# Optimization experiments

Measured on AMD Instinct MI355X. Metric: run time of the kernel, lower is better.

Reference implementation:

```python
import jax, jax.numpy as jnp
import numpy as np

LN_EPS = 1e-5


def setup_inputs() -> dict:
    key = jax.random.key(0)
    ks = jax.random.split(key, 4)
    B, S, D, V, M = 32, 512, 1024, 32000, 77
    X = jax.random.normal(ks[0], (B, S, D), dtype=jnp.float32)
    masked_positions = jax.random.randint(ks[1], (B, M), 0, S, dtype=jnp.int64 if jax.config.jax_enable_x64 else jnp.int32)
    W1 = jax.random.normal(ks[2], (D, D), dtype=jnp.float32) * (1.0 / np.sqrt(D))
    b1 = jnp.zeros((D,), jnp.float32)
    gamma = jnp.ones((D,), jnp.float32)
    beta = jnp.zeros((D,), jnp.float32)
    W2 = jax.random.normal(ks[3], (D, V), dtype=jnp.float32) * (1.0 / np.sqrt(D))
    b2 = jnp.zeros((V,), jnp.float32)
    return {"X": X, "masked_positions": masked_positions, "W1": W1, "b1": b1,
            "gamma": gamma, "beta": beta, "W2": W2, "b2": b2}


def reference(X, masked_positions, W1, b1, gamma, beta, W2, b2):
    # Gather masked token embeddings: X[b, masked_positions[b, m]] -> [B, M, D]
    masked_X = jnp.take_along_axis(X, masked_positions[:, :, None], axis=1)
    # Linear -> ReLU
    h = jax.nn.relu(jnp.einsum('bmd,dh->bmh', masked_X, W1) + b1)
    # LayerNorm over last dim
    mu = jnp.mean(h, axis=-1, keepdims=True)
    var = jnp.mean(jnp.square(h - mu), axis=-1, keepdims=True)
    h = (h - mu) * jax.lax.rsqrt(var + LN_EPS) * gamma + beta
    # Vocab projection
    return jnp.einsum('bmh,hv->bmv', h, W2) + b2
```

## Files before the change

kernel.cpp:

```cpp
#include <hip/hip_runtime.h>
#include <cstdint>

#define D_DIM 1024
#define V_DIM 32000
#define S_DIM 512
#define M_TOK 77
#define ROWS 2464
#define ROWS_PAD 2560

typedef __attribute__((ext_vector_type(8))) short bf16x8;
typedef __attribute__((ext_vector_type(4))) float f32x4;
typedef __attribute__((ext_vector_type(4))) uint16_t u16x4;

__device__ __forceinline__ uint16_t f2bf(float f) {
    union { float f; uint32_t u; } w; w.f = f;
    uint32_t r = (w.u + 0x7FFFu + ((w.u >> 16) & 1u)) >> 16;
    return (uint16_t)r;
}

__device__ __forceinline__ void async_copy16(const uint16_t* g, uint16_t* l) {
    __builtin_amdgcn_global_load_lds((const __attribute__((address_space(1))) void*)g,
                                     (__attribute__((address_space(3))) void*)l,
                                     16, 0, 0);
}

__global__ __launch_bounds__(256) void transpose_f32_bf16(const float* __restrict__ in,
                                                          uint16_t* __restrict__ out,
                                                          int R, int C) {
    __shared__ uint16_t tile[64][65];
    const int c0 = blockIdx.x * 64, r0 = blockIdx.y * 64;
    const int t  = threadIdx.x;
    const int lr = t >> 4;
    const int lc = (t & 15) * 4;
#pragma unroll
    for (int p = 0; p < 4; ++p) {
        const float* src = in + (size_t)(r0 + p * 16 + lr) * C + c0 + lc;
        f32x4 v = *(const f32x4*)src;
        tile[p * 16 + lr][lc + 0] = f2bf(v.x);
        tile[p * 16 + lr][lc + 1] = f2bf(v.y);
        tile[p * 16 + lr][lc + 2] = f2bf(v.z);
        tile[p * 16 + lr][lc + 3] = f2bf(v.w);
    }
    __syncthreads();
#pragma unroll
    for (int p = 0; p < 4; ++p) {
        const int oc = p * 16 + lr;
        u16x4 v;
        v.x = tile[lc + 0][oc];
        v.y = tile[lc + 1][oc];
        v.z = tile[lc + 2][oc];
        v.w = tile[lc + 3][oc];
        *(u16x4*)(out + (size_t)(c0 + oc) * R + r0 + lc) = v;
    }
}

__global__ __launch_bounds__(256) void gather_rows(const float* __restrict__ X,
                                                   const int* __restrict__ pos,
                                                   uint16_t* __restrict__ Ag) {
    const int r = blockIdx.x;
    const int t = threadIdx.x;
    size_t src = 0;
    if (r < ROWS) {
        const int b = r / M_TOK;
        const int p = pos[r];
        src = ((size_t)b * S_DIM + p) * D_DIM;
    }
    f32x4 v = *(const f32x4*)(X + src + t * 4);
    u16x4 o;
    o.x = f2bf(v.x); o.y = f2bf(v.y); o.z = f2bf(v.z); o.w = f2bf(v.w);
    *(u16x4*)(Ag + (size_t)r * D_DIM + t * 4) = o;
}

template <int EPI>
__global__ __launch_bounds__(256, 2) void gemm_bt(const uint16_t* __restrict__ A,
                                                  const uint16_t* __restrict__ B,
                                                  const float* __restrict__ bias,
                                                  float* __restrict__ C,
                                                  int K, int N, int MValid) {
    __shared__ uint16_t As[128 * 64];
    __shared__ uint16_t Bs[128 * 64];
    const int tid  = threadIdx.x;
    const int lane = tid & 63;
    const int wave = tid >> 6;
    const int wr   = (wave >> 1) * 64;
    const int wc   = (wave & 1) * 64;
    const int tM   = blockIdx.y * 128;
    const int tN   = blockIdx.x * 128;
    const int l15  = lane & 15;
    const int l4   = lane >> 4;

    const f32x4 zero = {0.f, 0.f, 0.f, 0.f};
    f32x4 acc[4][4];
#pragma unroll
    for (int i = 0; i < 4; ++i)
#pragma unroll
        for (int j = 0; j < 4; ++j) acc[i][j] = zero;

    const uint16_t* Agp = A + (size_t)(tM + (tid >> 3)) * K + (tid & 7) * 8;
    const uint16_t* Bgp = B + (size_t)(tN + (tid >> 3)) * K + (tid & 7) * 8;
    uint16_t* Asl = &As[tid * 8];
    uint16_t* Bsl = &Bs[tid * 8];
    const size_t rstep = (size_t)32 * K;

    for (int k0 = 0; k0 < K; k0 += 64) {
#pragma unroll
        for (int i = 0; i < 4; ++i)
            async_copy16(Agp + i * rstep + k0, Asl + i * 2048);
#pragma unroll
        for (int i = 0; i < 4; ++i)
            async_copy16(Bgp + i * rstep + k0, Bsl + i * 2048);
        __syncthreads();
#pragma unroll
        for (int kk = 0; kk < 2; ++kk) {
            bf16x8 af[4], bfr[4];
#pragma unroll
            for (int i = 0; i < 4; ++i)
                af[i] = *(const bf16x8*)&As[(wr + i * 16 + l15) * 64 + kk * 32 + l4 * 8];
#pragma unroll
            for (int j = 0; j < 4; ++j)
                bfr[j] = *(const bf16x8*)&Bs[(wc + j * 16 + l15) * 64 + kk * 32 + l4 * 8];
#pragma unroll
            for (int i = 0; i < 4; ++i)
#pragma unroll
                for (int j = 0; j < 4; ++j)
                    acc[i][j] = __builtin_amdgcn_mfma_f32_16x16x32_bf16(af[i], bfr[j],
                                                                        acc[i][j], 0, 0, 0);
        }
        __syncthreads();
    }

#pragma unroll
    for (int j = 0; j < 4; ++j) {
        const int col = tN + wc + j * 16 + l15;
        const float bv = bias[col];
#pragma unroll
        for (int i = 0; i < 4; ++i) {
            const int row0 = tM + wr + i * 16 + l4 * 4;
#pragma unroll
            for (int r = 0; r < 4; ++r) {
                const int row = row0 + r;
                float v = acc[i][j][r] + bv;
                if (EPI == 0) {
                    v = v > 0.f ? v : 0.f;
                    C[(size_t)row * N + col] = v;
                } else {
                    if (row < MValid)
                        C[(size_t)row * N + col] = v;
                }
            }
        }
    }
}

__global__ __launch_bounds__(256) void layernorm_rows(const float* __restrict__ H,
                                                      const float* __restrict__ gamma,
                                                      const float* __restrict__ beta,
                                                      uint16_t* __restrict__ Hn) {
    const int row = blockIdx.x;
    const int t   = threadIdx.x;
    const float* h = H + (size_t)row * D_DIM;
    f32x4 v = *(const f32x4*)(h + t * 4);
    float s  = v.x + v.y + v.z + v.w;
    float sq = v.x * v.x + v.y * v.y + v.z * v.z + v.w * v.w;
#pragma unroll
    for (int o = 32; o > 0; o >>= 1) {
        s  += __shfl_down(s, o, 64);
        sq += __shfl_down(sq, o, 64);
    }
    __shared__ float ss[4], sqs[4];
    if ((t & 63) == 0) { ss[t >> 6] = s; sqs[t >> 6] = sq; }
    __syncthreads();
    const float S    = ss[0] + ss[1] + ss[2] + ss[3];
    const float SQ   = sqs[0] + sqs[1] + sqs[2] + sqs[3];
    const float mean = S * (1.f / D_DIM);
    const float var  = SQ * (1.f / D_DIM) - mean * mean;
    const float rstd = rsqrtf(var + 1e-5f);
    const int c = t * 4;
    f32x4 g = *(const f32x4*)(gamma + c);
    f32x4 bt = *(const f32x4*)(beta + c);
    u16x4 o;
    o.x = f2bf((v.x - mean) * rstd * g.x + bt.x);
    o.y = f2bf((v.y - mean) * rstd * g.y + bt.y);
    o.z = f2bf((v.z - mean) * rstd * g.z + bt.z);
    o.w = f2bf((v.w - mean) * rstd * g.w + bt.w);
    *(u16x4*)(Hn + (size_t)row * D_DIM + c) = o;
}

extern "C" void kernel_launch(void* const* d_in, const int* in_sizes, int n_in,
                              void* d_out, int out_size, void* d_ws, size_t ws_size,
                              hipStream_t stream) {
    const float* X     = (const float*)d_in[0];
    const int*   mp    = (const int*)d_in[1];
    const float* W1    = (const float*)d_in[2];
    const float* b1    = (const float*)d_in[3];
    const float* gamma = (const float*)d_in[4];
    const float* beta  = (const float*)d_in[5];
    const float* W2    = (const float*)d_in[6];
    const float* b2    = (const float*)d_in[7];

    char* ws = (char*)d_ws;
    uint16_t* W2T = (uint16_t*)(ws);
    uint16_t* W1T = (uint16_t*)(ws + 65536000);
    uint16_t* Ag  = (uint16_t*)(ws + 65536000 + 2097152);
    uint16_t* Hn  = (uint16_t*)(ws + 65536000 + 2097152 + 5242880);
    float*    H   = (float*)   (ws + 65536000 + 2097152 + 5242880 + 5242880);

    transpose_f32_bf16<<<dim3(V_DIM / 64, D_DIM / 64), 256, 0, stream>>>(W2, W2T, D_DIM, V_DIM);
    transpose_f32_bf16<<<dim3(D_DIM / 64, D_DIM / 64), 256, 0, stream>>>(W1, W1T, D_DIM, D_DIM);
    gather_rows<<<ROWS_PAD, 256, 0, stream>>>(X, mp, Ag);
    gemm_bt<0><<<dim3(D_DIM / 128, ROWS_PAD / 128), 256, 0, stream>>>(Ag, W1T, b1, H,
                                                                      D_DIM, D_DIM, ROWS_PAD);
    layernorm_rows<<<ROWS_PAD, 256, 0, stream>>>(H, gamma, beta, Hn);
    gemm_bt<1><<<dim3(V_DIM / 128, ROWS_PAD / 128), 256, 0, stream>>>(Hn, W2T, b2, (float*)d_out,
                                                                      D_DIM, V_DIM, ROWS);
}
```

Baseline: 712.9 us.

## Replace vocab GEMM with 256x256 double-buffered, swizzled, XCD-remapped MFMA kernel

Adds a dedicated kernel for the large vocab projection. It uses 256x256 tiles with 8 waves and double-buffered LDS, so global-to-LDS loads of the next K step overlap the current MFMAs. It also adds an XOR swizzle to avoid LDS bank conflicts, remaps workgroups across XCDs for cache locality, and uses setprio around the MFMA bursts. The trade-offs are heavy register pressure (128 accumulator floats per lane) and 128KB of LDS per block, which limits occupancy. The larger tiles also waste more work on padded rows and leave fewer workgroups overall (1250).

Result: faster. 690.6 us (-3.1%).

```diff
diff --git a/kernel.cpp b/kernel.cpp
--- a/kernel.cpp
+++ b/kernel.cpp
@@ -7,6 +7,14 @@
 #define M_TOK 77
 #define ROWS 2464
 #define ROWS_PAD 2560
+
+#define G2_BM 256
+#define G2_BN 256
+#define G2_BK 64
+#define G2_MT (ROWS_PAD / G2_BM)
+#define G2_NT (V_DIM / G2_BN)
+#define G2_NWG (G2_MT * G2_NT)
+#define G2_KT (D_DIM / G2_BK)
 
 typedef __attribute__((ext_vector_type(8))) short bf16x8;
 typedef __attribute__((ext_vector_type(4))) float f32x4;
@@ -152,6 +160,154 @@
     }
 }
 
+__global__ __launch_bounds__(512, 2) void gemm2_256(const uint16_t* __restrict__ A,
+                                                    const uint16_t* __restrict__ B,
+                                                    const float* __restrict__ bias,
+                                                    float* __restrict__ C,
+                                                    int MValid) {
+    __shared__ uint16_t lds[65536];
+    const int tid  = threadIdx.x;
+    const int lane = tid & 63;
+    const int wave = tid >> 6;
+    const int l15  = lane & 15;
+    const int l4   = lane >> 4;
+    const int R0   = (wave >> 2) * 128;
+    const int C0   = (wave & 3) * 64;
+
+    const int bid = blockIdx.x;
+    const int q = G2_NWG >> 3, r = G2_NWG & 7;
+    const int xcd = bid & 7, lin = bid >> 3;
+    const int wg = (xcd < r ? xcd * (q + 1) : r * (q + 1) + (xcd - r) * q) + lin;
+    const int tM = (wg % G2_MT) * G2_BM;
+    const int tN = (wg / G2_MT) * G2_BN;
+
+    const int srow = tid >> 3;
+    const int scel = ((((tid & 7) << 4) ^ ((srow & 7) << 4)) >> 1);
+    const uint16_t* Ags = A + (size_t)(tM + srow) * D_DIM + scel;
+    const uint16_t* Bgs = B + (size_t)(tN + srow) * D_DIM + scel;
+    uint16_t* AsD = &lds[tid * 8];
+    uint16_t* BsD = &lds[16384 + tid * 8];
+
+    const f32x4 zero = {0.f, 0.f, 0.f, 0.f};
+    f32x4 acc[8][4];
+#pragma unroll
+    for (int i = 0; i < 8; ++i)
+#pragma unroll
+        for (int j = 0; j < 4; ++j) acc[i][j] = zero;
+
+    const int colk0 = (l4 * 8) ^ ((l15 & 7) << 3);
+    const int colk1 = colk0 ^ 32;
+
+#pragma unroll
+    for (int i = 0; i < 4; ++i)
+        async_copy16(Ags + (size_t)(i * 64) * D_DIM, AsD + i * 4096);
+#pragma unroll
+    for (int i = 0; i < 4; ++i)
+        async_copy16(Bgs + (size_t)(i * 64) * D_DIM, BsD + i * 4096);
+    asm volatile("s_waitcnt vmcnt(0)" ::: "memory");
+    __builtin_amdgcn_s_barrier();
+
+#pragma unroll 2
+    for (int t = 0; t < G2_KT; ++t) {
+        const int bA = (t & 1) << 15;
+        const int bB = bA + 16384;
+        bf16x8 af[4], bf[4];
+
+#pragma unroll
+        for (int i = 0; i < 4; ++i)
+            af[i] = *(const bf16x8*)&lds[bA + (R0 + i * 16 + l15) * 64 + colk0];
+#pragma unroll
+        for (int j = 0; j < 4; ++j)
+            bf[j] = *(const bf16x8*)&lds[bB + (C0 + j * 16 + l15) * 64 + colk0];
+        if (t + 1 < G2_KT) {
+            const int k0 = (t + 1) * G2_BK;
+            const int sb = bA ^ 32768;
+#pragma unroll
+            for (int i = 0; i < 4; ++i)
+                async_copy16(Ags + (size_t)(i * 64) * D_DIM + k0, AsD + sb + i * 4096);
+#pragma unroll
+            for (int i = 0; i < 4; ++i)
+                async_copy16(Bgs + (size_t)(i * 64) * D_DIM + k0, BsD + sb + i * 4096);
+        }
+        __builtin_amdgcn_s_barrier();
+        asm volatile("s_waitcnt lgkmcnt(0)" ::: "memory");
+        __builtin_amdgcn_s_setprio(1);
+#pragma unroll
+        for (int i = 0; i < 4; ++i)
+#pragma unroll
+            for (int j = 0; j < 4; ++j)
+                acc[i][j] = __builtin_amdgcn_mfma_f32_16x16x32_bf16(af[i], bf[j],
+                                                                    acc[i][j], 0, 0, 0);
+        __builtin_amdgcn_s_setprio(0);
+        __builtin_amdgcn_s_barrier();
+
+#pragma unroll
+        for (int i = 0; i < 4; ++i)
+            af[i] = *(const bf16x8*)&lds[bA + (R0 + 64 + i * 16 + l15) * 64 + colk0];
+        __builtin_amdgcn_s_barrier();
+        asm volatile("s_waitcnt lgkmcnt(0)" ::: "memory");
+        __builtin_amdgcn_s_setprio(1);
+#pragma unroll
+        for (int i = 0; i < 4; ++i)
+#pragma unroll
+            for (int j = 0; j < 4; ++j)
+                acc[4 + i][j] = __builtin_amdgcn_mfma_f32_16x16x32_bf16(af[i], bf[j],
+                                                                        acc[4 + i][j], 0, 0, 0);
+        __builtin_amdgcn_s_setprio(0);
+        __builtin_amdgcn_s_barrier();
+
+#pragma unroll
+        for (int i = 0; i < 4; ++i)
+            af[i] = *(const bf16x8*)&lds[bA + (R0 + i * 16 + l15) * 64 + colk1];
+#pragma unroll
+        for (int j = 0; j < 4; ++j)
+            bf[j] = *(const bf16x8*)&lds[bB + (C0 + j * 16 + l15) * 64 + colk1];
+        __builtin_amdgcn_s_barrier();
+        asm volatile("s_waitcnt lgkmcnt(0)" ::: "memory");
+        __builtin_amdgcn_s_setprio(1);
+#pragma unroll
+        for (int i = 0; i < 4; ++i)
+#pragma unroll
+            for (int j = 0; j < 4; ++j)
+                acc[i][j] = __builtin_amdgcn_mfma_f32_16x16x32_bf16(af[i], bf[j],
+                                                                    acc[i][j], 0, 0, 0);
+        __builtin_amdgcn_s_setprio(0);
+        __builtin_amdgcn_s_barrier();
+
+#pragma unroll
+        for (int i = 0; i < 4; ++i)
+            af[i] = *(const bf16x8*)&lds[bA + (R0 + 64 + i * 16 + l15) * 64 + colk1];
+        __builtin_amdgcn_s_barrier();
+        asm volatile("s_waitcnt lgkmcnt(0)" ::: "memory");
+        __builtin_amdgcn_s_setprio(1);
+#pragma unroll
+        for (int i = 0; i < 4; ++i)
+#pragma unroll
+            for (int j = 0; j < 4; ++j)
+                acc[4 + i][j] = __builtin_amdgcn_mfma_f32_16x16x32_bf16(af[i], bf[j],
+                                                                        acc[4 + i][j], 0, 0, 0);
+        __builtin_amdgcn_s_setprio(0);
+        asm volatile("s_waitcnt vmcnt(0)" ::: "memory");
+        __builtin_amdgcn_s_barrier();
+    }
+
+#pragma unroll
+    for (int j = 0; j < 4; ++j) {
+        const int col = tN + C0 + j * 16 + l15;
+        const float bv = bias[col];
+#pragma unroll
+        for (int i = 0; i < 8; ++i) {
+            const int row0 = tM + R0 + i * 16 + l4 * 4;
+#pragma unroll
+            for (int rr = 0; rr < 4; ++rr) {
+                const int row = row0 + rr;
+                if (row < MValid)
+                    C[(size_t)row * V_DIM + col] = acc[i][j][rr] + bv;
+            }
+        }
+    }
+}
+
 __global__ __launch_bounds__(256) void layernorm_rows(const float* __restrict__ H,
                                                       const float* __restrict__ gamma,
                                                       const float* __restrict__ beta,
@@ -211,6 +367,5 @@
     gemm_bt<0><<<dim3(D_DIM / 128, ROWS_PAD / 128), 256, 0, stream>>>(Ag, W1T, b1, H,
                                                                       D_DIM, D_DIM, ROWS_PAD);
     layernorm_rows<<<ROWS_PAD, 256, 0, stream>>>(H, gamma, beta, Hn);
-    gemm_bt<1><<<dim3(V_DIM / 128, ROWS_PAD / 128), 256, 0, stream>>>(Hn, W2T, b2, (float*)d_out,
-                                                                      D_DIM, V_DIM, ROWS);
-}
+    gemm2_256<<<dim3(G2_NWG), 512, 0, stream>>>(Hn, W2T, b2, (float*)d_out, ROWS);
+}
```

## Replace vocab GEMM with 256x256 four-stage pipelined kernel with XCD remap

Applied to the files above, without the earlier changes.

Replaces the second GEMM (2560x1024 by 1024x32000) with a new kernel that uses 256x256 tiles, 8 waves, a 4-deep LDS ring buffer of BK=32 stages filled by async global-to-LDS copies, XOR-swizzled LDS layout, s_setprio around MFMA bursts, and a workgroup-to-XCD remapping for L2 locality. It aims to raise arithmetic intensity and hide global-load latency, which the old single-buffered 128x128 kernel exposed. The costs are 128 KB of LDS per block, which limits occupancy, 128 accumulator registers per thread, and hand-managed waitcnt/barrier sequencing that could be fragile.

New measurement: 693.3 us. 1.03x faster.

```diff
diff --git a/kernel.cpp b/kernel.cpp
--- a/kernel.cpp
+++ b/kernel.cpp
@@ -7,6 +7,14 @@
 #define M_TOK 77
 #define ROWS 2464
 #define ROWS_PAD 2560
+
+#define G2_BM 256
+#define G2_BN 256
+#define G2_BK 32
+#define G2_MT (ROWS_PAD / G2_BM)
+#define G2_NT (V_DIM / G2_BN)
+#define G2_NWG (G2_MT * G2_NT)
+#define G2_KT (D_DIM / G2_BK)
 
 typedef __attribute__((ext_vector_type(8))) short bf16x8;
 typedef __attribute__((ext_vector_type(4))) float f32x4;
@@ -152,6 +160,121 @@
     }
 }
 
+#define G2_TILE(T, STAGE, VM)                                                              \
+    do {                                                                                   \
+        asm volatile("s_waitcnt vmcnt(" #VM ")" ::: "memory");                             \
+        __builtin_amdgcn_s_barrier();                                                      \
+        const int bufc = ((T) & 3) * 16384;                                                \
+        bf16x8 af[4], bfv[4];                                                              \
+        _Pragma("unroll") for (int i = 0; i < 4; ++i)                                      \
+            af[i] = *(const bf16x8*)&lds[bufc + (R0 + i * 16 + l15) * 32 + swr];           \
+        _Pragma("unroll") for (int j = 0; j < 4; ++j)                                      \
+            bfv[j] = *(const bf16x8*)&lds[bufc + 8192 + (C0 + j * 16 + l15) * 32 + swr];   \
+        if (STAGE) {                                                                       \
+            const int sb = (((T) + 3) & 3) * 16384;                                        \
+            const int k0 = ((T) + 3) * G2_BK;                                              \
+            async_copy16(Ag0 + k0, AsD + sb);                                              \
+            async_copy16(Ag1 + k0, AsD + sb + 4096);                                       \
+            async_copy16(Bg0 + k0, BsD + sb);                                              \
+            async_copy16(Bg1 + k0, BsD + sb + 4096);                                       \
+        }                                                                                  \
+        __builtin_amdgcn_s_barrier();                                                      \
+        asm volatile("s_waitcnt lgkmcnt(0)" ::: "memory");                                 \
+        __builtin_amdgcn_s_setprio(1);                                                     \
+        _Pragma("unroll") for (int i = 0; i < 4; ++i)                                      \
+            _Pragma("unroll") for (int j = 0; j < 4; ++j)                                  \
+                acc[i][j] = __builtin_amdgcn_mfma_f32_16x16x32_bf16(af[i], bfv[j],         \
+                                                                    acc[i][j], 0, 0, 0);   \
+        __builtin_amdgcn_s_setprio(0);                                                     \
+        __builtin_amdgcn_s_barrier();                                                      \
+        _Pragma("unroll") for (int i = 0; i < 4; ++i)                                      \
+            af[i] = *(const bf16x8*)&lds[bufc + (R0 + 64 + i * 16 + l15) * 32 + swr];      \
+        __builtin_amdgcn_s_barrier();                                                      \
+        asm volatile("s_waitcnt lgkmcnt(0)" ::: "memory");                                 \
+        __builtin_amdgcn_s_setprio(1);                                                     \
+        _Pragma("unroll") for (int i = 0; i < 4; ++i)                                      \
+            _Pragma("unroll") for (int j = 0; j < 4; ++j)                                  \
+                acc[4 + i][j] = __builtin_amdgcn_mfma_f32_16x16x32_bf16(af[i], bfv[j],     \
+                                                                        acc[4 + i][j],    \
+                                                                        0, 0, 0);          \
+        __builtin_amdgcn_s_setprio(0);                                                     \
+    } while (0)
+
+__global__ __launch_bounds__(512, 2) void gemm2_256(const uint16_t* __restrict__ A,
+                                                    const uint16_t* __restrict__ B,
+                                                    const float* __restrict__ bias,
+                                                    float* __restrict__ C,
+                                                    int MValid) {
+    __shared__ uint16_t lds[65536];
+    const int tid  = threadIdx.x;
+    const int lane = tid & 63;
+    const int wave = tid >> 6;
+    const int l15  = lane & 15;
+    const int l4   = lane >> 4;
+    const int R0   = (wave >> 2) * 128;
+    const int C0   = (wave & 3) * 64;
+
+    const int bid = blockIdx.x;
+    const int q = G2_NWG >> 3, r = G2_NWG & 7;
+    const int xcd = bid & 7, lin = bid >> 3;
+    const int wg = (xcd < r ? xcd * (q + 1) : r * (q + 1) + (xcd - r) * q) + lin;
+    const int tM = (wg % G2_MT) * G2_BM;
+    const int tN = (wg / G2_MT) * G2_BN;
+
+    const int srow  = tid >> 2;
+    const int sslot = tid & 3;
+    const int swcol = ((sslot ^ ((srow >> 1) & 3)) << 3);
+    const uint16_t* Ag0 = A + (size_t)(tM + srow) * D_DIM + swcol;
+    const uint16_t* Ag1 = Ag0 + (size_t)128 * D_DIM;
+    const uint16_t* Bg0 = B + (size_t)(tN + srow) * D_DIM + swcol;
+    const uint16_t* Bg1 = Bg0 + (size_t)128 * D_DIM;
+    uint16_t* AsD = &lds[tid * 8];
+    uint16_t* BsD = &lds[8192 + tid * 8];
+
+    const int swr = ((l4 ^ ((l15 >> 1) & 3)) << 3);
+
+    const f32x4 zero = {0.f, 0.f, 0.f, 0.f};
+    f32x4 acc[8][4];
+#pragma unroll
+    for (int i = 0; i < 8; ++i)
+#pragma unroll
+        for (int j = 0; j < 4; ++j) acc[i][j] = zero;
+
+#pragma unroll
+    for (int t = 0; t < 3; ++t) {
+        const int sb = t * 16384;
+        const int k0 = t * G2_BK;
+        async_copy16(Ag0 + k0, AsD + sb);
+        async_copy16(Ag1 + k0, AsD + sb + 4096);
+        async_copy16(Bg0 + k0, BsD + sb);
+        async_copy16(Bg1 + k0, BsD + sb + 4096);
+    }
+
+#pragma unroll 2
+    for (int T = 0; T < G2_KT - 3; ++T) {
+        G2_TILE(T, true, 8);
+    }
+    G2_TILE(G2_KT - 3, false, 8);
+    G2_TILE(G2_KT - 2, false, 4);
+    G2_TILE(G2_KT - 1, false, 0);
+
+#pragma unroll
+    for (int j = 0; j < 4; ++j) {
+        const int col = tN + C0 + j * 16 + l15;
+        const float bv = bias[col];
+#pragma unroll
+        for (int i = 0; i < 8; ++i) {
+            const int row0 = tM + R0 + i * 16 + l4 * 4;
+#pragma unroll
+            for (int rr = 0; rr < 4; ++rr) {
+                const int row = row0 + rr;
+                if (row < MValid)
+                    C[(size_t)row * V_DIM + col] = acc[i][j][rr] + bv;
+            }
+        }
+    }
+}
+
 __global__ __launch_bounds__(256) void layernorm_rows(const float* __restrict__ H,
                                                       const float* __restrict__ gamma,
                                                       const float* __restrict__ beta,
@@ -211,6 +334,5 @@
     gemm_bt<0><<<dim3(D_DIM / 128, ROWS_PAD / 128), 256, 0, stream>>>(Ag, W1T, b1, H,
                                                                       D_DIM, D_DIM, ROWS_PAD);
     layernorm_rows<<<ROWS_PAD, 256, 0, stream>>>(H, gamma, beta, Hn);
-    gemm_bt<1><<<dim3(V_DIM / 128, ROWS_PAD / 128), 256, 0, stream>>>(Hn, W2T, b2, (float*)d_out,
-                                                                      D_DIM, V_DIM, ROWS);
-}
+    gemm2_256<<<dim3(G2_NWG), 512, 0, stream>>>(Hn, W2T, b2, (float*)d_out, ROWS);
+}
```

## Replace vocab GEMM with 256x256 double-buffered pipelined MFMA kernel

Applied to the files above, without the earlier changes.

Replaces the 128x128 vocab projection GEMM with a new 512-thread kernel using 256x256 tiles. The kernel double-buffers LDS with async global-to-LDS copies staged across sub-phases, applies an XOR swizzle to avoid bank conflicts, raises wave priority around the MFMA blocks, and remaps workgroups per XCD for L2 locality. The goal is more data reuse per tile and overlap of loads with compute. In exchange it uses 128KB of LDS and many more accumulator registers, and its fixed 2560x32000 tiling leaves some tail waste (32000/256 = 125 column tiles).

New measurement: 690.9 us. 3.1% less time.

```diff
diff --git a/kernel.cpp b/kernel.cpp
--- a/kernel.cpp
+++ b/kernel.cpp
@@ -7,6 +7,14 @@
 #define M_TOK 77
 #define ROWS 2464
 #define ROWS_PAD 2560
+
+#define G2_BM 256
+#define G2_BN 256
+#define G2_BK 64
+#define G2_MT (ROWS_PAD / G2_BM)
+#define G2_NT (V_DIM / G2_BN)
+#define G2_NWG (G2_MT * G2_NT)
+#define G2_KT (D_DIM / G2_BK)
 
 typedef __attribute__((ext_vector_type(8))) short bf16x8;
 typedef __attribute__((ext_vector_type(4))) float f32x4;
@@ -152,6 +160,128 @@
     }
 }
 
+#define G2B(T) (((T) & 1) * 32768)
+#define BAR    __builtin_amdgcn_s_barrier()
+#define LGKM0  asm volatile("s_waitcnt lgkmcnt(0)" ::: "memory")
+
+#define RD_FA(T, H)                                                                         \
+    _Pragma("unroll") for (int i = 0; i < 4; ++i) {                                         \
+        fa[i * 2 + 0] = *(const bf16x8*)&lds[G2B(T) + (R0 + (H) * 64 + i * 16 + l15) * 64 + colk0]; \
+        fa[i * 2 + 1] = *(const bf16x8*)&lds[G2B(T) + (R0 + (H) * 64 + i * 16 + l15) * 64 + colk1]; \
+    }
+
+#define RD_FB(T, FB, J0)                                                                    \
+    _Pragma("unroll") for (int j = 0; j < 2; ++j) {                                         \
+        FB[j * 2 + 0] = *(const bf16x8*)&lds[G2B(T) + 16384 + (C0 + ((J0) + j) * 16 + l15) * 64 + colk0]; \
+        FB[j * 2 + 1] = *(const bf16x8*)&lds[G2B(T) + 16384 + (C0 + ((J0) + j) * 16 + l15) * 64 + colk1]; \
+    }
+
+#define STG(T, G)                                                                 \
+    do {                                                                          \
+        const int sb_ = G2B(T);                                                   \
+        async_copy16(Ags + (size_t)(G) * 64 * D_DIM + (T) * G2_BK, AsD + sb_ + (G) * 4096); \
+        async_copy16(Bgs + (size_t)(G) * 64 * D_DIM + (T) * G2_BK, BsD + sb_ + (G) * 4096); \
+    } while (0)
+
+#define MM(H, JP, FB)                                                                       \
+    __builtin_amdgcn_s_setprio(1);                                                          \
+    _Pragma("unroll") for (int i = 0; i < 4; ++i)                                           \
+    _Pragma("unroll") for (int j = 0; j < 2; ++j)                                           \
+    _Pragma("unroll") for (int kk = 0; kk < 2; ++kk)                                        \
+        acc[(H) * 4 + i][(JP) * 2 + j] =                                                    \
+            __builtin_amdgcn_mfma_f32_16x16x32_bf16(fa[i * 2 + kk], FB[j * 2 + kk],         \
+                                                    acc[(H) * 4 + i][(JP) * 2 + j], 0, 0, 0); \
+    __builtin_amdgcn_s_setprio(0);
+
+#define KTILE(T, S1, S2, VM)                                  \
+    do {                                                      \
+                                       \
+        RD_FA(T, 0); RD_FB(T, fbA, 0);                        \
+        if (S1) STG((T) + 1, 1);                              \
+        BAR; LGKM0; MM(0, 0, fbA); BAR;                       \
+                                       \
+        RD_FB(T, fbB, 2);                                     \
+        if (S1) STG((T) + 1, 2);                              \
+        BAR; LGKM0; MM(0, 1, fbB); BAR;                       \
+                                       \
+        RD_FA(T, 1);                                          \
+        if (S1) STG((T) + 1, 3);                              \
+        BAR; LGKM0; MM(1, 0, fbA); BAR;                       \
+         \
+        if (S2) STG((T) + 2, 0);                              \
+        asm volatile("s_waitcnt vmcnt(" #VM ")" ::: "memory"); \
+        BAR; MM(1, 1, fbB); BAR;                              \
+    } while (0)
+
+__global__ __launch_bounds__(512, 2) void gemm2_256(const uint16_t* __restrict__ A,
+                                                    const uint16_t* __restrict__ B,
+                                                    const float* __restrict__ bias,
+                                                    float* __restrict__ C,
+                                                    int MValid) {
+    __shared__ uint16_t lds[65536];
+    const int tid  = threadIdx.x;
+    const int lane = tid & 63;
+    const int wave = tid >> 6;
+    const int l15  = lane & 15;
+    const int l4   = lane >> 4;
+    const int R0   = (wave >> 2) * 128;
+    const int C0   = (wave & 3) * 64;
+
+    const int bid = blockIdx.x;
+    const int q = G2_NWG >> 3, r = G2_NWG & 7;
+    const int xcd = bid & 7, lin = bid >> 3;
+    const int wg = (xcd < r ? xcd * (q + 1) : r * (q + 1) + (xcd - r) * q) + lin;
+    const int tM = (wg % G2_MT) * G2_BM;
+    const int tN = (wg / G2_MT) * G2_BN;
+
+    const int srow  = tid >> 3;
+    const int swcol = (((tid & 7) ^ (srow & 7)) << 3);
+    const uint16_t* Ags = A + (size_t)(tM + srow) * D_DIM + swcol;
+    const uint16_t* Bgs = B + (size_t)(tN + srow) * D_DIM + swcol;
+    uint16_t* AsD = &lds[tid * 8];
+    uint16_t* BsD = &lds[16384 + tid * 8];
+
+    const int colk0 = (l4 * 8) ^ ((l15 & 7) << 3);
+    const int colk1 = colk0 ^ 32;
+
+    const f32x4 zero = {0.f, 0.f, 0.f, 0.f};
+    f32x4 acc[8][4];
+#pragma unroll
+    for (int i = 0; i < 8; ++i)
+#pragma unroll
+        for (int j = 0; j < 4; ++j) acc[i][j] = zero;
+
+    bf16x8 fa[8], fbA[4], fbB[4];
+
+#pragma unroll
+    for (int g = 0; g < 4; ++g) STG(0, g);
+    STG(1, 0);
+    asm volatile("s_waitcnt vmcnt(2)" ::: "memory");
+    BAR;
+
+#pragma unroll 2
+    for (int T = 0; T < G2_KT - 2; ++T)
+        KTILE(T, 1, 1, 2);
+    KTILE(14, 1, 0, 0);
+    KTILE(15, 0, 0, 0);
+
+#pragma unroll
+    for (int j = 0; j < 4; ++j) {
+        const int col = tN + C0 + j * 16 + l15;
+        const float bv = bias[col];
+#pragma unroll
+        for (int i = 0; i < 8; ++i) {
+            const int row0 = tM + R0 + i * 16 + l4 * 4;
+#pragma unroll
+            for (int rr = 0; rr < 4; ++rr) {
+                const int row = row0 + rr;
+                if (row < MValid)
+                    C[(size_t)row * V_DIM + col] = acc[i][j][rr] + bv;
+            }
+        }
+    }
+}
+
 __global__ __launch_bounds__(256) void layernorm_rows(const float* __restrict__ H,
                                                       const float* __restrict__ gamma,
                                                       const float* __restrict__ beta,
@@ -211,6 +341,5 @@
     gemm_bt<0><<<dim3(D_DIM / 128, ROWS_PAD / 128), 256, 0, stream>>>(Ag, W1T, b1, H,
                                                                       D_DIM, D_DIM, ROWS_PAD);
     layernorm_rows<<<ROWS_PAD, 256, 0, stream>>>(H, gamma, beta, Hn);
-    gemm_bt<1><<<dim3(V_DIM / 128, ROWS_PAD / 128), 256, 0, stream>>>(Hn, W2T, b2, (float*)d_out,
-                                                                      D_DIM, V_DIM, ROWS);
-}
+    gemm2_256<<<dim3(G2_NWG), 512, 0, stream>>>(Hn, W2T, b2, (float*)d_out, ROWS);
+}
```
